# Performance work log

Measured on AMD Instinct MI355X. Metric: run time of the kernel, lower is better.

The kernel has to match this reference:

```python
import jax, jax.numpy as jnp
import numpy as np

N = 1200        # nodes in the (complete) graph
SLOPE = 0.1     # leaky_relu negative slope
# smat: 10-vector -> symmetric 4x4
SMAT_IDX = np.array([0,1,2,3,1,4,5,6,2,5,7,8,3,6,8,9])

def _glorot(k, shape):
    lim = float(np.sqrt(6.0 / (shape[0] + shape[1])))
    return jax.random.uniform(k, shape, jnp.float32, -lim, lim)

def setup_inputs():
    key = jax.random.key(0)
    ks = jax.random.split(key, 24)
    # complete graph connectivity (recover_S reads edge_map[i,j] for all i!=j)
    iu, ju = np.triu_indices(N, k=1)
    E = iu.shape[0]
    eid = np.arange(E, dtype=np.int32)
    edge_map = np.zeros((N, N), dtype=np.int32)
    edge_map[iu, ju] = eid
    edge_map[ju, iu] = eid
    ud_edges = np.stack([iu, ju], axis=1).astype(np.int32)           # [E,2]
    edge_index = np.stack([np.concatenate([iu, ju]),
                           np.concatenate([ju, iu])]).astype(np.int32)  # [2,2E]
    inp = {
        'x': jax.random.normal(ks[0], (N, 16), jnp.float32),
        'edge_index': jnp.asarray(edge_index),
        'edge_map': jnp.asarray(edge_map),
        'ud_edges': jnp.asarray(ud_edges),
    }
    dims = {'g': [(6, 32), (32, 32), (32, 64)],
            'n': [(64, 64), (64, 64), (64, 10)],
            'e': [(64, 64), (64, 64), (64, 16)]}
    k = 1
    for tag, ds in dims.items():
        for i, (a, b) in enumerate(ds):
            inp[f'W{tag}{i+1}'] = _glorot(ks[k], (a, b)); k += 1
            inp[f'b{tag}{i+1}'] = jnp.zeros((b,), jnp.float32)
    return inp

def _leaky(v):
    return jnp.where(v >= 0, v, SLOPE * v)

def _gcn(x, src, dst, W, b):
    deg = jax.ops.segment_sum(jnp.ones(src.shape[0], x.dtype), dst, num_segments=N)
    dinv = jnp.where(deg > 0, jax.lax.rsqrt(deg), 0.0)
    norm = dinv[src] * dinv[dst]
    h = x @ W
    return jax.ops.segment_sum(norm[:, None] * h[src], dst, num_segments=N) + b

def _mlp3(h, W1, b1, W2, b2, W3, b3):
    # dropout is identity (eval mode)
    h = _leaky(h @ W1 + b1)
    h = _leaky(h @ W2 + b2)
    return h @ W3 + b3

def _forward(x, edge_index, edge_map, ud_edges,
             Wg1, bg1, Wg2, bg2, Wg3, bg3,
             Wn1, bn1, Wn2, bn2, Wn3, bn3,
             We1, be1, We2, be2, We3, be3):
    x6 = x[:, 0:6]                       # node_feature_mode == 1
    src, dst = edge_index[0], edge_index[1]
    h = _leaky(_gcn(x6, src, dst, Wg1, bg1))
    h = _leaky(_gcn(h, src, dst, Wg2, bg2))
    h = _gcn(h, src, dst, Wg3, bg3)      # [N,64]
    vd = _mlp3(h, Wn1, bn1, Wn2, bn2, Wn3, bn3)            # [N,10]
    he = h[ud_edges[:, 0]] + h[ud_edges[:, 1]]             # [E,64]
    ed = _mlp3(he, We1, be1, We2, be2, We3, be3)           # [E,16]
    # recover_S: block-structured [4N,4N]
    Vsym = vd[:, jnp.asarray(SMAT_IDX)].reshape(N, 4, 4)   # smat per node
    Eb = ed.reshape(-1, 4, 4)
    B = Eb[edge_map]                                       # [N,N,4,4]
    ii = jnp.arange(N)
    lower = ii[:, None] > ii[None, :]
    B = jnp.where(lower[:, :, None, None], jnp.swapaxes(B, 2, 3), B)
    B = B.at[ii, ii].set(Vsym)
    S = B.transpose(0, 2, 1, 3).reshape(4 * N, 4 * N)
    return h, S

def reference(x, edge_index, edge_map, ud_edges,
              Wg1, bg1, Wg2, bg2, Wg3, bg3,
              Wn1, bn1, Wn2, bn2, Wn3, bn3,
              We1, be1, We2, be2, We3, be3):
    return _forward(x, edge_index, edge_map, ud_edges,
                    Wg1, bg1, Wg2, bg2, Wg3, bg3,
                    Wn1, bn1, Wn2, bn2, Wn3, bn3,
                    We1, be1, We2, be2, We3, be3)
```

## Files before the change

### kernel.cpp

```cpp
#include <hip/hip_runtime.h>

#define NN 1200
#define NE 719400
#define SDIM 4800

typedef __attribute__((ext_vector_type(8))) short bf16x8;
typedef __attribute__((ext_vector_type(4))) short bf16x4;
typedef __attribute__((ext_vector_type(4))) float f32x4;

static __device__ __constant__ int SMAT[16] = {0,1,2,3,1,4,5,6,2,5,7,8,3,6,8,9};

__device__ __forceinline__ float lk(float v) { return v >= 0.f ? v : 0.1f * v; }

#if __has_builtin(__builtin_amdgcn_mfma_f32_16x16x16bf16_1k)
__device__ __forceinline__ f32x4 mfma1616(bf16x4 a, bf16x4 b, f32x4 c) {
    return __builtin_amdgcn_mfma_f32_16x16x16bf16_1k(a, b, c, 0, 0, 0);
}
#else
__device__ __forceinline__ f32x4 mfma1616(bf16x4 a, bf16x4 b, f32x4 c) {
    asm volatile("v_mfma_f32_16x16x16_bf16 %0, %1, %2, %0\n\ts_nop 7\n\ts_nop 7"
                 : "+v"(c) : "v"(a), "v"(b));
    return c;
}
#endif

__device__ __forceinline__ void split8(const float* u, bf16x8& hi, bf16x8& lo) {
#pragma unroll
    for (int e = 0; e < 8; e++) {
        unsigned x = __float_as_uint(u[e]);
        unsigned r = x + 0x7FFFu + ((x >> 16) & 1u);
        hi[e] = (short)(r >> 16);
        float hf = __uint_as_float(r & 0xFFFF0000u);
        float s = u[e] - hf;
        unsigned v = __float_as_uint(s);
        unsigned w = v + 0x7FFFu + ((v >> 16) & 1u);
        lo[e] = (short)(w >> 16);
    }
}

__device__ __forceinline__ void split4(const float* u, bf16x4& hi, bf16x4& lo) {
#pragma unroll
    for (int e = 0; e < 4; e++) {
        unsigned x = __float_as_uint(u[e]);
        unsigned r = x + 0x7FFFu + ((x >> 16) & 1u);
        hi[e] = (short)(r >> 16);
        float hf = __uint_as_float(r & 0xFFFF0000u);
        float s = u[e] - hf;
        unsigned v = __float_as_uint(s);
        unsigned w = v + 0x7FFFu + ((v >> 16) & 1u);
        lo[e] = (short)(w >> 16);
    }
}

__device__ __forceinline__ uint2 split2(float a0, float a1) {
    unsigned u0 = __float_as_uint(a0), u1 = __float_as_uint(a1);
    unsigned r0 = u0 + 0x7FFFu + ((u0 >> 16) & 1u);
    unsigned r1 = u1 + 0x7FFFu + ((u1 >> 16) & 1u);
    float h0 = __uint_as_float(r0 & 0xFFFF0000u);
    float h1 = __uint_as_float(r1 & 0xFFFF0000u);
    float s0 = a0 - h0, s1 = a1 - h1;
    unsigned v0 = __float_as_uint(s0), v1 = __float_as_uint(s1);
    unsigned t0 = v0 + 0x7FFFu + ((v0 >> 16) & 1u);
    unsigned t1 = v1 + 0x7FFFu + ((v1 >> 16) & 1u);
    unsigned hi = (r0 >> 16) | (r1 & 0xFFFF0000u);
    unsigned lo = (t0 >> 16) | (t1 & 0xFFFF0000u);
    return make_uint2(hi, lo);
}

__global__ void k_prep(const float* __restrict__ We2, const float* __restrict__ We3,
                       unsigned* __restrict__ W2F, unsigned* __restrict__ W3F,
                       float* __restrict__ cs) {
    int t = blockIdx.x * 256 + threadIdx.x;
    if (t < 512) {
        int lane = t & 63, ks = (t >> 6) & 1, mt = t >> 7;
        int m = mt * 16 + (lane & 15);
        int kb = ks * 32 + (lane >> 4) * 8;
        unsigned hi[4], lo[4];
#pragma unroll
        for (int p = 0; p < 4; p++) {
            float a0 = We2[(kb + 2 * p) * 64 + m];
            float a1 = We2[(kb + 2 * p + 1) * 64 + m];
            uint2 hl = split2(a0, a1);
            hi[p] = hl.x; lo[p] = hl.y;
        }
        *(uint4*)(W2F + ((mt * 2 + ks) * 2 + 0) * 256 + lane * 4) = make_uint4(hi[0], hi[1], hi[2], hi[3]);
        *(uint4*)(W2F + ((mt * 2 + ks) * 2 + 1) * 256 + lane * 4) = make_uint4(lo[0], lo[1], lo[2], lo[3]);
    } else if (t < 768) {
        int q = t - 512;
        int lane = q & 63, kb = q >> 6;
        int c = lane & 15;
        int k0 = kb * 16 + (lane >> 4) * 4;
        unsigned hi[2], lo[2];
#pragma unroll
        for (int p = 0; p < 2; p++) {
            float a0 = We3[(k0 + 2 * p) * 16 + c];
            float a1 = We3[(k0 + 2 * p + 1) * 16 + c];
            uint2 hl = split2(a0, a1);
            hi[p] = hl.x; lo[p] = hl.y;
        }
        *(uint2*)(W3F + (kb * 2 + 0) * 128 + lane * 2) = make_uint2(hi[0], hi[1]);
        *(uint2*)(W3F + (kb * 2 + 1) * 128 + lane * 2) = make_uint2(lo[0], lo[1]);
    } else if (t < 896) {
        cs[t - 768] = 0.f;
    }
}

__global__ __launch_bounds__(256) void k_t1(const float* __restrict__ x,
                                            const float* __restrict__ Wg1,
                                            float* __restrict__ t1,
                                            float* __restrict__ cs1) {
    int T = blockIdx.x * 256 + threadIdx.x;
    int c = T & 31, rs = T >> 5;
    float w[6];
#pragma unroll
    for (int k = 0; k < 6; k++) w[k] = Wg1[k * 32 + c];
    float loc = 0.f;
    for (int r = rs; r < NN; r += 304) {
        float acc = 0.f;
#pragma unroll
        for (int k = 0; k < 6; k++) acc = fmaf(x[r * 16 + k], w[k], acc);
        t1[r * 32 + c] = acc;
        loc += acc;
    }
    atomicAdd(&cs1[c], loc);
}

__global__ __launch_bounds__(256) void k_t2(const float* __restrict__ t1,
                                            const float* __restrict__ cs1,
                                            const float* __restrict__ bg1,
                                            const float* __restrict__ Wg2,
                                            float* __restrict__ t2,
                                            float* __restrict__ cs2) {
    int T = blockIdx.x * 256 + threadIdx.x;
    int c = T & 31, rs = T >> 5;
    const float inv = 1.0f / 1199.0f;
    float p[32], w[32];
#pragma unroll
    for (int k = 0; k < 32; k++) {
        p[k] = fmaf(cs1[k], inv, bg1[k]);
        w[k] = Wg2[k * 32 + c];
    }
    float loc = 0.f;
    for (int r = rs; r < NN; r += 304) {
        float acc = 0.f;
#pragma unroll
        for (int k = 0; k < 32; k++) {
            float h = lk(fmaf(-t1[r * 32 + k], inv, p[k]));
            acc = fmaf(h, w[k], acc);
        }
        t2[r * 32 + c] = acc;
        loc += acc;
    }
    atomicAdd(&cs2[c], loc);
}

__global__ __launch_bounds__(256) void k_t3(const float* __restrict__ t2,
                                            const float* __restrict__ cs2,
                                            const float* __restrict__ bg2,
                                            const float* __restrict__ Wg3,
                                            float* __restrict__ t3,
                                            float* __restrict__ cs3) {
    int T = blockIdx.x * 256 + threadIdx.x;
    int c = T & 63, rs = T >> 6;
    const float inv = 1.0f / 1199.0f;
    float p[32], w[32];
#pragma unroll
    for (int k = 0; k < 32; k++) {
        p[k] = fmaf(cs2[k], inv, bg2[k]);
        w[k] = Wg3[k * 64 + c];
    }
    float loc = 0.f;
    for (int r = rs; r < NN; r += 152) {
        float acc = 0.f;
#pragma unroll
        for (int k = 0; k < 32; k++) {
            float h = lk(fmaf(-t2[r * 32 + k], inv, p[k]));
            acc = fmaf(h, w[k], acc);
        }
        t3[r * 64 + c] = acc;
        loc += acc;
    }
    atomicAdd(&cs3[c], loc);
}

__global__ __launch_bounds__(256) void k_g(const float* __restrict__ t3,
                                           const float* __restrict__ cs3,
                                           const float* __restrict__ bg3,
                                           const float* __restrict__ We1,
                                           float* __restrict__ h_out,
                                           float* __restrict__ g_out) {
    __shared__ float H[32][65];
    __shared__ float W[4096];
    const int tid = threadIdx.x;
    const int r0 = blockIdx.x * 32;
    const float inv = 1.0f / 1199.0f;

    for (int t = tid; t < 1024; t += 256) ((float4*)W)[t] = ((const float4*)We1)[t];
    for (int t = tid; t < 2048; t += 256) {
        int i = t >> 6, c = t & 63;
        int row = r0 + i;
        float v = 0.f;
        if (row < NN) {
            v = fmaf(cs3[c] - t3[row * 64 + c], inv, bg3[c]);
            h_out[row * 64 + c] = v;
        }
        H[i][c] = v;
    }
    __syncthreads();

    int rg = tid >> 3, cg = tid & 7;
    float acc[8] = {};
#pragma unroll 8
    for (int k = 0; k < 64; k++) {
        float a = H[rg][k];
        float4 b0 = *(const float4*)&W[k * 64 + cg * 8];
        float4 b1 = *(const float4*)&W[k * 64 + cg * 8 + 4];
        acc[0] = fmaf(a, b0.x, acc[0]); acc[1] = fmaf(a, b0.y, acc[1]);
        acc[2] = fmaf(a, b0.z, acc[2]); acc[3] = fmaf(a, b0.w, acc[3]);
        acc[4] = fmaf(a, b1.x, acc[4]); acc[5] = fmaf(a, b1.y, acc[5]);
        acc[6] = fmaf(a, b1.z, acc[6]); acc[7] = fmaf(a, b1.w, acc[7]);
    }
    int row = r0 + rg;
    if (row < NN) {
        *(float4*)&g_out[row * 64 + cg * 8]     = make_float4(acc[0], acc[1], acc[2], acc[3]);
        *(float4*)&g_out[row * 64 + cg * 8 + 4] = make_float4(acc[4], acc[5], acc[6], acc[7]);
    }
}

__global__ __launch_bounds__(256) void k_vd(const float* __restrict__ h,
                                            const float* __restrict__ Wn1, const float* __restrict__ bn1,
                                            const float* __restrict__ Wn2, const float* __restrict__ bn2,
                                            const float* __restrict__ Wn3, const float* __restrict__ bn3,
                                            float* __restrict__ S) {
    __shared__ float H[32][65];
    __shared__ float N1[32][65];
    __shared__ float WB[4096];
    __shared__ float WC[4096];
    __shared__ float WD[640];
    __shared__ float VD[32][12];
    __shared__ float sb1[64], sb2[64], sb3[16];

    const int tid = threadIdx.x;
    const int r0 = blockIdx.x * 32;

    for (int t = tid; t < 1024; t += 256) {
        ((float4*)WB)[t] = ((const float4*)Wn1)[t];
        ((float4*)WC)[t] = ((const float4*)Wn2)[t];
    }
    for (int t = tid; t < 640; t += 256) WD[t] = Wn3[t];
    if (tid < 64) { sb1[tid] = bn1[tid]; sb2[tid] = bn2[tid]; }
    if (tid < 10) sb3[tid] = bn3[tid];

    for (int t = tid; t < 2048; t += 256) {
        int i = t >> 6, c = t & 63;
        int row = r0 + i;
        H[i][c] = (row < NN) ? h[row * 64 + c] : 0.f;
    }
    __syncthreads();

    int rg = tid >> 3, cg = tid & 7;
    {
        float acc[8] = {};
#pragma unroll 8
        for (int k = 0; k < 64; k++) {
            float a = H[rg][k];
            float4 b0 = *(const float4*)&WB[k * 64 + cg * 8];
            float4 b1 = *(const float4*)&WB[k * 64 + cg * 8 + 4];
            acc[0] = fmaf(a, b0.x, acc[0]); acc[1] = fmaf(a, b0.y, acc[1]);
            acc[2] = fmaf(a, b0.z, acc[2]); acc[3] = fmaf(a, b0.w, acc[3]);
            acc[4] = fmaf(a, b1.x, acc[4]); acc[5] = fmaf(a, b1.y, acc[5]);
            acc[6] = fmaf(a, b1.z, acc[6]); acc[7] = fmaf(a, b1.w, acc[7]);
        }
#pragma unroll
        for (int q = 0; q < 8; q++) N1[rg][cg * 8 + q] = lk(acc[q] + sb1[cg * 8 + q]);
    }
    __syncthreads();
    {
        float acc[8] = {};
#pragma unroll 8
        for (int k = 0; k < 64; k++) {
            float a = N1[rg][k];
            float4 b0 = *(const float4*)&WC[k * 64 + cg * 8];
            float4 b1 = *(const float4*)&WC[k * 64 + cg * 8 + 4];
            acc[0] = fmaf(a, b0.x, acc[0]); acc[1] = fmaf(a, b0.y, acc[1]);
            acc[2] = fmaf(a, b0.z, acc[2]); acc[3] = fmaf(a, b0.w, acc[3]);
            acc[4] = fmaf(a, b1.x, acc[4]); acc[5] = fmaf(a, b1.y, acc[5]);
            acc[6] = fmaf(a, b1.z, acc[6]); acc[7] = fmaf(a, b1.w, acc[7]);
        }
#pragma unroll
        for (int q = 0; q < 8; q++) H[rg][cg * 8 + q] = lk(acc[q] + sb2[cg * 8 + q]);
    }
    __syncthreads();
    for (int t = tid; t < 320; t += 256) {
        int r = t / 10, c = t % 10;
        float acc = sb3[c];
        for (int k = 0; k < 64; k++) acc = fmaf(H[r][k], WD[k * 10 + c], acc);
        VD[r][c] = acc;
    }
    __syncthreads();
    if (tid < 128) {
        int r = tid >> 2, a = tid & 3;
        int row = r0 + r;
        if (row < NN) {
            float4 v = make_float4(VD[r][SMAT[a * 4 + 0]], VD[r][SMAT[a * 4 + 1]],
                                   VD[r][SMAT[a * 4 + 2]], VD[r][SMAT[a * 4 + 3]]);
            *(float4*)&S[(4 * row + a) * SDIM + 4 * row] = v;
        }
    }
}

__global__ __launch_bounds__(256) void k_edge(const int* __restrict__ ud,
                                              const float* __restrict__ g,
                                              const float* __restrict__ be1,
                                              const float* __restrict__ be2,
                                              const float* __restrict__ be3,
                                              const unsigned* __restrict__ W2F,
                                              const unsigned* __restrict__ W3F,
                                              float* __restrict__ S) {
    __shared__ float EDW[4][32][17];

    const int tid = threadIdx.x;
    const int wave = tid >> 6, lane = tid & 63;
    const int lrow = lane & 15, lgrp = lane >> 4;
    const int base_e = blockIdx.x * 128 + wave * 32;

    const int e0 = base_e + lrow;
    const int e1 = base_e + 16 + lrow;
    const int2 ij0 = ((const int2*)ud)[min(e0, NE - 1)];
    const int2 ij1 = ((const int2*)ud)[min(e1, NE - 1)];

    f32x4 b1a[2][2];
#pragma unroll
    for (int ks = 0; ks < 2; ks++) {
        b1a[ks][0] = *(const f32x4*)(be1 + ks * 32 + lgrp * 8);
        b1a[ks][1] = *(const f32x4*)(be1 + ks * 32 + lgrp * 8 + 4);
    }

    bf16x8 Uhi[2][2], Ulo[2][2];
#pragma unroll
    for (int nt = 0; nt < 2; nt++) {
        const int2 ij = nt ? ij1 : ij0;
        const float* gi = g + ij.x * 64;
        const float* gj = g + ij.y * 64;
#pragma unroll
        for (int ks = 0; ks < 2; ks++) {
            int kb = ks * 32 + lgrp * 8;
            f32x4 x0 = *(const f32x4*)(gi + kb);
            f32x4 x1 = *(const f32x4*)(gi + kb + 4);
            f32x4 y0 = *(const f32x4*)(gj + kb);
            f32x4 y1 = *(const f32x4*)(gj + kb + 4);
            float u[8];
#pragma unroll
            for (int e = 0; e < 4; e++) {
                u[e]     = lk(x0[e] + y0[e] + b1a[ks][0][e]);
                u[4 + e] = lk(x1[e] + y1[e] + b1a[ks][1][e]);
            }
            split8(u, Uhi[nt][ks], Ulo[nt][ks]);
        }
    }

    bf16x4 Vhi[4][2], Vlo[4][2];
#pragma unroll
    for (int mt = 0; mt < 4; mt++) {
        f32x4 acc[2];
#pragma unroll
        for (int nt = 0; nt < 2; nt++)
#pragma unroll
            for (int q = 0; q < 4; q++) acc[nt][q] = 0.f;
#pragma unroll
        for (int ks = 0; ks < 2; ks++) {
            bf16x8 Whi = *(const bf16x8*)(W2F + ((mt * 2 + ks) * 2 + 0) * 256 + lane * 4);
            bf16x8 Wlo = *(const bf16x8*)(W2F + ((mt * 2 + ks) * 2 + 1) * 256 + lane * 4);
#pragma unroll
            for (int nt = 0; nt < 2; nt++) {
                acc[nt] = __builtin_amdgcn_mfma_f32_16x16x32_bf16(Whi, Uhi[nt][ks], acc[nt], 0, 0, 0);
                acc[nt] = __builtin_amdgcn_mfma_f32_16x16x32_bf16(Wlo, Uhi[nt][ks], acc[nt], 0, 0, 0);
                acc[nt] = __builtin_amdgcn_mfma_f32_16x16x32_bf16(Whi, Ulo[nt][ks], acc[nt], 0, 0, 0);
            }
        }
        f32x4 b2 = *(const f32x4*)(be2 + mt * 16 + lgrp * 4);
#pragma unroll
        for (int nt = 0; nt < 2; nt++) {
            float v[4];
#pragma unroll
            for (int q = 0; q < 4; q++) v[q] = lk(acc[nt][q] + b2[q]);
            split4(v, Vhi[mt][nt], Vlo[mt][nt]);
        }
    }

    f32x4 acc3[2];
#pragma unroll
    for (int nt = 0; nt < 2; nt++)
#pragma unroll
        for (int q = 0; q < 4; q++) acc3[nt][q] = 0.f;
#pragma unroll
    for (int kb = 0; kb < 4; kb++) {
        bf16x4 W3h = *(const bf16x4*)(W3F + (kb * 2 + 0) * 128 + lane * 2);
        bf16x4 W3l = *(const bf16x4*)(W3F + (kb * 2 + 1) * 128 + lane * 2);
#pragma unroll
        for (int nt = 0; nt < 2; nt++) {
            acc3[nt] = mfma1616(W3h, Vhi[kb][nt], acc3[nt]);
            acc3[nt] = mfma1616(W3l, Vhi[kb][nt], acc3[nt]);
            acc3[nt] = mfma1616(W3h, Vlo[kb][nt], acc3[nt]);
        }
    }

    f32x4 b3 = *(const f32x4*)(be3 + lgrp * 4);
#pragma unroll
    for (int nt = 0; nt < 2; nt++) {
        const int e = nt ? e1 : e0;
        const int2 ij = nt ? ij1 : ij0;
        float ed[4];
#pragma unroll
        for (int q = 0; q < 4; q++) {
            ed[q] = acc3[nt][q] + b3[q];
            EDW[wave][nt * 16 + lrow][lgrp * 4 + q] = ed[q];
        }
        if (e < NE) {
            *(float4*)&S[(4 * ij.x + lgrp) * SDIM + 4 * ij.y] =
                make_float4(ed[0], ed[1], ed[2], ed[3]);
        }
    }

    const int le = lane & 31;
    const int lg2 = lane >> 5;
    const int eL = base_e + le;
    const int2 ijL = ((const int2*)ud)[min(eL, NE - 1)];
#pragma unroll
    for (int q = 0; q < 2; q++) {
        int a = lg2 * 2 + q;
        float4 v = make_float4(EDW[wave][le][a], EDW[wave][le][4 + a],
                               EDW[wave][le][8 + a], EDW[wave][le][12 + a]);
        if (eL < NE) *(float4*)&S[(4 * ijL.y + a) * SDIM + 4 * ijL.x] = v;
    }
}

extern "C" void kernel_launch(void* const* d_in, const int* in_sizes, int n_in,
                              void* d_out, int out_size, void* d_ws, size_t ws_size,
                              hipStream_t stream) {
    const float* x   = (const float*)d_in[0];
    const int*   ud  = (const int*)d_in[3];
    const float* Wg1 = (const float*)d_in[4];
    const float* bg1 = (const float*)d_in[5];
    const float* Wg2 = (const float*)d_in[6];
    const float* bg2 = (const float*)d_in[7];
    const float* Wg3 = (const float*)d_in[8];
    const float* bg3 = (const float*)d_in[9];
    const float* Wn1 = (const float*)d_in[10];
    const float* bn1 = (const float*)d_in[11];
    const float* Wn2 = (const float*)d_in[12];
    const float* bn2 = (const float*)d_in[13];
    const float* Wn3 = (const float*)d_in[14];
    const float* bn3 = (const float*)d_in[15];
    const float* We1 = (const float*)d_in[16];
    const float* be1 = (const float*)d_in[17];
    const float* We2 = (const float*)d_in[18];
    const float* be2 = (const float*)d_in[19];
    const float* We3 = (const float*)d_in[20];
    const float* be3 = (const float*)d_in[21];

    float* out   = (float*)d_out;
    float* h_out = out;
    float* S     = out + 76800;

    float* ws  = (float*)d_ws;
    float* t1  = ws;
    float* t2  = ws + 38400;
    float* t3  = ws + 76800;
    float* g   = ws + 153600;
    float* cs  = ws + 230400;
    unsigned* W2F = (unsigned*)(ws + 230528);
    unsigned* W3F = W2F + 4096;

    k_prep<<<4, 256, 0, stream>>>(We2, We3, W2F, W3F, cs);
    k_t1<<<38, 256, 0, stream>>>(x, Wg1, t1, cs);
    k_t2<<<38, 256, 0, stream>>>(t1, cs, bg1, Wg2, t2, cs + 32);
    k_t3<<<38, 256, 0, stream>>>(t2, cs + 32, bg2, Wg3, t3, cs + 64);
    k_g<<<38, 256, 0, stream>>>(t3, cs + 64, bg3, We1, h_out, g);
    k_edge<<<5621, 256, 0, stream>>>(ud, g, be1, be2, be3, W2F, W3F, S);
    k_vd<<<38, 256, 0, stream>>>(h_out, Wn1, bn1, Wn2, bn2, Wn3, bn3, S);
}
```

Measured before the change: 125.3 us.

## Stage edge outputs in workspace and write transposed lower blocks in a coalesced pass

The edge kernel now writes each edge's 4x4 output to a contiguous workspace buffer instead of scattering transposed blocks into the lower triangle of S. A new kernel walks the lower triangle one row J at a time, reads the buffered blocks and writes contiguous rows of S, which should coalesce those stores. This costs an extra write and read of about 46 MB of edge data plus one more launch. The path is only used when the workspace is large enough, so it may not run at all.

```diff
diff --git a/kernel.cpp b/kernel.cpp
--- a/kernel.cpp
+++ b/kernel.cpp
@@ -316,7 +316,9 @@
                                               const float* __restrict__ be3,
                                               const unsigned* __restrict__ W2F,
                                               const unsigned* __restrict__ W3F,
-                                              float* __restrict__ S) {
+                                              float* __restrict__ S,
+                                              float* __restrict__ ed_buf,
+                                              int use_buf) {
     __shared__ float EDW[4][32][17];
 
     const int tid = threadIdx.x;
@@ -419,19 +421,48 @@
         if (e < NE) {
             *(float4*)&S[(4 * ij.x + lgrp) * SDIM + 4 * ij.y] =
                 make_float4(ed[0], ed[1], ed[2], ed[3]);
-        }
-    }
-
-    const int le = lane & 31;
-    const int lg2 = lane >> 5;
-    const int eL = base_e + le;
-    const int2 ijL = ((const int2*)ud)[min(eL, NE - 1)];
-#pragma unroll
-    for (int q = 0; q < 2; q++) {
-        int a = lg2 * 2 + q;
-        float4 v = make_float4(EDW[wave][le][a], EDW[wave][le][4 + a],
-                               EDW[wave][le][8 + a], EDW[wave][le][12 + a]);
-        if (eL < NE) *(float4*)&S[(4 * ijL.y + a) * SDIM + 4 * ijL.x] = v;
+            if (use_buf)
+                *(float4*)&ed_buf[e * 16 + lgrp * 4] =
+                    make_float4(ed[0], ed[1], ed[2], ed[3]);
+        }
+    }
+
+    if (!use_buf) {
+        const int le = lane & 31;
+        const int lg2 = lane >> 5;
+        const int eL = base_e + le;
+        const int2 ijL = ((const int2*)ud)[min(eL, NE - 1)];
+#pragma unroll
+        for (int q = 0; q < 2; q++) {
+            int a = lg2 * 2 + q;
+            float4 v = make_float4(EDW[wave][le][a], EDW[wave][le][4 + a],
+                                   EDW[wave][le][8 + a], EDW[wave][le][12 + a]);
+            if (eL < NE) *(float4*)&S[(4 * ijL.y + a) * SDIM + 4 * ijL.x] = v;
+        }
+    }
+}
+
+__global__ __launch_bounds__(256) void k_low(const float* __restrict__ ed_buf,
+                                             float* __restrict__ S) {
+    const int tid = threadIdx.x;
+#pragma unroll
+    for (int rep = 0; rep < 2; rep++) {
+        const int J = rep ? (NN - 1 - (int)blockIdx.x) : (int)blockIdx.x;
+        for (int i0 = 0; i0 < J; i0 += 256) {
+            int i = i0 + tid;
+            if (i < J) {
+                int e = i * (NN - 1) - (i * (i + 1)) / 2 + (J - i - 1);
+                const float* eb = ed_buf + e * 16;
+                f32x4 q0 = *(const f32x4*)(eb);
+                f32x4 q1 = *(const f32x4*)(eb + 4);
+                f32x4 q2 = *(const f32x4*)(eb + 8);
+                f32x4 q3 = *(const f32x4*)(eb + 12);
+                *(float4*)&S[(4 * J + 0) * SDIM + 4 * i] = make_float4(q0[0], q1[0], q2[0], q3[0]);
+                *(float4*)&S[(4 * J + 1) * SDIM + 4 * i] = make_float4(q0[1], q1[1], q2[1], q3[1]);
+                *(float4*)&S[(4 * J + 2) * SDIM + 4 * i] = make_float4(q0[2], q1[2], q2[2], q3[2]);
+                *(float4*)&S[(4 * J + 3) * SDIM + 4 * i] = make_float4(q0[3], q1[3], q2[3], q3[3]);
+            }
+        }
     }
 }
 
@@ -471,12 +502,17 @@
     float* cs  = ws + 230400;
     unsigned* W2F = (unsigned*)(ws + 230528);
     unsigned* W3F = W2F + 4096;
+    float* ed_buf = ws + 235648;
+
+    const size_t need = (size_t)(235648 + (size_t)NE * 16) * 4;
+    const int use_buf = (ws_size >= need) ? 1 : 0;
 
     k_prep<<<4, 256, 0, stream>>>(We2, We3, W2F, W3F, cs);
     k_t1<<<38, 256, 0, stream>>>(x, Wg1, t1, cs);
     k_t2<<<38, 256, 0, stream>>>(t1, cs, bg1, Wg2, t2, cs + 32);
     k_t3<<<38, 256, 0, stream>>>(t2, cs + 32, bg2, Wg3, t3, cs + 64);
     k_g<<<38, 256, 0, stream>>>(t3, cs + 64, bg3, We1, h_out, g);
-    k_edge<<<5621, 256, 0, stream>>>(ud, g, be1, be2, be3, W2F, W3F, S);
+    k_edge<<<5621, 256, 0, stream>>>(ud, g, be1, be2, be3, W2F, W3F, S, ed_buf, use_buf);
+    if (use_buf) k_low<<<600, 256, 0, stream>>>(ed_buf, S);
     k_vd<<<38, 256, 0, stream>>>(h_out, Wn1, bn1, Wn2, bn2, Wn3, bn3, S);
 }
```

Result: slower. 139.8 us (+11.5%).

## Move lower-triangle transposed writes from edge kernel into separate tiled transpose kernel

Applied to the files above, without the earlier changes.

The edge kernel now writes only the upper-triangle 4x4 blocks of S. A new kernel reads 64x64 tiles from the upper triangle through shared memory and writes their transposes into the lower triangle, so those scattered per-edge stores become coalesced. This costs an extra launch and a full re-read of half of S (about 46 MB) in exchange for replacing uncoalesced scattered writes.

```diff
diff --git a/kernel.cpp b/kernel.cpp
--- a/kernel.cpp
+++ b/kernel.cpp
@@ -317,8 +317,6 @@
                                               const unsigned* __restrict__ W2F,
                                               const unsigned* __restrict__ W3F,
                                               float* __restrict__ S) {
-    __shared__ float EDW[4][32][17];
-
     const int tid = threadIdx.x;
     const int wave = tid >> 6, lane = tid & 63;
     const int lrow = lane & 15, lgrp = lane >> 4;
@@ -410,28 +408,45 @@
     for (int nt = 0; nt < 2; nt++) {
         const int e = nt ? e1 : e0;
         const int2 ij = nt ? ij1 : ij0;
-        float ed[4];
-#pragma unroll
-        for (int q = 0; q < 4; q++) {
-            ed[q] = acc3[nt][q] + b3[q];
-            EDW[wave][nt * 16 + lrow][lgrp * 4 + q] = ed[q];
-        }
         if (e < NE) {
             *(float4*)&S[(4 * ij.x + lgrp) * SDIM + 4 * ij.y] =
-                make_float4(ed[0], ed[1], ed[2], ed[3]);
-        }
-    }
-
-    const int le = lane & 31;
-    const int lg2 = lane >> 5;
-    const int eL = base_e + le;
-    const int2 ijL = ((const int2*)ud)[min(eL, NE - 1)];
-#pragma unroll
-    for (int q = 0; q < 2; q++) {
-        int a = lg2 * 2 + q;
-        float4 v = make_float4(EDW[wave][le][a], EDW[wave][le][4 + a],
-                               EDW[wave][le][8 + a], EDW[wave][le][12 + a]);
-        if (eL < NE) *(float4*)&S[(4 * ijL.y + a) * SDIM + 4 * ijL.x] = v;
+                make_float4(acc3[nt][0] + b3[0], acc3[nt][1] + b3[1],
+                            acc3[nt][2] + b3[2], acc3[nt][3] + b3[3]);
+        }
+    }
+}
+
+__global__ __launch_bounds__(256) void k_tr(float* __restrict__ S) {
+    __shared__ float T[64][65];
+    const int tid = threadIdx.x;
+
+    int b = blockIdx.x;
+    int ti = 0;
+    while (b >= 75 - ti) { b -= 75 - ti; ti++; }
+    const int tj = ti + b;
+    const int r0 = ti * 64, c0 = tj * 64;
+
+#pragma unroll
+    for (int it = 0; it < 4; ++it) {
+        int idx = tid + it * 256;
+        int rr = idx >> 4, cc4 = idx & 15;
+        float4 v = *(const float4*)&S[(r0 + rr) * SDIM + c0 + cc4 * 4];
+        T[rr][cc4 * 4 + 0] = v.x; T[rr][cc4 * 4 + 1] = v.y;
+        T[rr][cc4 * 4 + 2] = v.z; T[rr][cc4 * 4 + 3] = v.w;
+    }
+    __syncthreads();
+
+#pragma unroll
+    for (int it = 0; it < 4; ++it) {
+        int idx = tid + it * 256;
+        int cc = idx >> 4, rr4 = idx & 15;
+        int br = (r0 >> 2) + rr4;
+        int bc = (c0 >> 2) + (cc >> 2);
+        if (bc > br) {
+            float4 w = make_float4(T[rr4 * 4 + 0][cc], T[rr4 * 4 + 1][cc],
+                                   T[rr4 * 4 + 2][cc], T[rr4 * 4 + 3][cc]);
+            *(float4*)&S[(c0 + cc) * SDIM + r0 + rr4 * 4] = w;
+        }
     }
 }
 
@@ -478,5 +493,6 @@
     k_t3<<<38, 256, 0, stream>>>(t2, cs + 32, bg2, Wg3, t3, cs + 64);
     k_g<<<38, 256, 0, stream>>>(t3, cs + 64, bg3, We1, h_out, g);
     k_edge<<<5621, 256, 0, stream>>>(ud, g, be1, be2, be3, W2F, W3F, S);
+    k_tr<<<2850, 256, 0, stream>>>(S);
     k_vd<<<38, 256, 0, stream>>>(h_out, Wn1, bn1, Wn2, bn2, Wn3, bn3, S);
 }
```

Result: slower. 132.3 us (+5.5%).
